# Optimization experiments

Measured on AMD Instinct MI355X. Metric: run time of the kernel, lower is better.

The kernel has to match this reference:

```python
import jax, jax.numpy as jnp
import numpy as np

H = 32          # num_attention_heads
HD = 128        # head_dim
HID = H * HD    # hidden_size = 4096
KB_LEN = 1024   # number of KB entries
TOPK = 128      # top_k_kb (dynamic_sparsify=True)
ROPE_THETA = 10000.0
PAD = -1000000000.0  # PADDING_VALUE


def rope_cos_sin(position_ids, head_dim, theta):
    inv_freq = 1.0 / (theta ** (jnp.arange(0, head_dim, 2, dtype=jnp.float32) / head_dim))
    freqs = position_ids.astype(jnp.float32)[..., None] * inv_freq  # [B,q,hd/2]
    emb = jnp.concatenate([freqs, freqs], axis=-1)                  # [B,q,hd]
    return jnp.cos(emb), jnp.sin(emb)


def rotate_half(x):
    half = x.shape[-1] // 2
    return jnp.concatenate([-x[..., half:], x[..., :half]], axis=-1)


def apply_rope(q, k, cos, sin):
    cos = cos[:, None]  # [B,1,q,hd]
    sin = sin[:, None]
    return q * cos + rotate_half(q) * sin, k * cos + rotate_half(k) * sin


def setup_inputs() -> dict:
    key = jax.random.key(0)
    ks = jax.random.split(key, 9)
    B, Q = 1, 2048
    w_scale = 0.02  # keep activations numerically sane
    hidden_states = jax.random.normal(ks[0], (B, Q, HID), jnp.float32)
    causal = jnp.where(jnp.tril(jnp.ones((Q, Q), bool)), 0.0, PAD).astype(jnp.float32)
    attention_mask = jnp.broadcast_to(causal[None, None], (B, 1, Q, Q))
    position_ids = jnp.broadcast_to(jnp.arange(Q)[None], (B, Q))
    kb_keys = jax.random.normal(ks[1], (KB_LEN, HID), jnp.float32)
    kb_values = jax.random.normal(ks[2], (KB_LEN, HID), jnp.float32)
    Wq = jax.random.normal(ks[3], (HID, HID), jnp.float32) * w_scale
    Wq2 = jax.random.normal(ks[4], (HID, HID), jnp.float32) * w_scale
    Wk = jax.random.normal(ks[5], (HID, HID), jnp.float32) * w_scale
    Wv = jax.random.normal(ks[6], (HID, HID), jnp.float32) * w_scale
    Wo = jax.random.normal(ks[7], (HID, HID), jnp.float32) * w_scale
    score_shift = jnp.zeros((H, 1), jnp.float32) - 3.0
    return {"hidden_states": hidden_states, "attention_mask": attention_mask,
            "position_ids": position_ids, "kb_keys": kb_keys, "kb_values": kb_values,
            "Wq": Wq, "Wq2": Wq2, "Wk": Wk, "Wv": Wv, "Wo": Wo,
            "score_shift": score_shift}


def kblam_attention(hidden_states, attention_mask, position_ids, kb_keys, kb_values,
                    Wq, Wq2, Wk, Wv, Wo, score_shift):
    B, Q, _ = hidden_states.shape
    scale = 1.0 / np.sqrt(HD)

    def heads(x):  # [B,Q,HID] -> [B,H,Q,HD]
        return x.reshape(B, Q, H, HD).transpose(0, 2, 1, 3)

    q = heads(hidden_states @ Wq.T)
    q2 = heads(hidden_states @ Wq2.T)   # second query head (used for KB top-k pruning)
    k = heads(hidden_states @ Wk.T)
    v = heads(hidden_states @ Wv.T)

    cos, sin = rope_cos_sin(position_ids, HD, ROPE_THETA)
    q, k = apply_rope(q, k, cos, sin)   # num_kv_groups == 1, repeat_kv is identity

    # --- KB path: [kb_len, H*HD] -> [B,H,kb_len,HD] ---
    kbk = jnp.broadcast_to(kb_keys.reshape(KB_LEN, H, HD).transpose(1, 0, 2)[None], (B, H, KB_LEN, HD))
    kbv = jnp.broadcast_to(kb_values.reshape(KB_LEN, H, HD).transpose(1, 0, 2)[None], (B, H, KB_LEN, HD))

    # prune_key_value (dynamic_sparsify): top-k KB rows by summed q2-scores
    aw2 = jnp.einsum('bhqd,bhkd->bhqk', q2, kbk) * scale          # [B,H,Q,KB_LEN]
    idx = jax.lax.stop_gradient(jax.lax.top_k(aw2.sum((1, 2)), TOPK)[1])  # [B,TOPK]
    gidx = jnp.broadcast_to(idx[:, None, :, None], (B, H, TOPK, HD))
    kbk = jnp.take_along_axis(kbk, gidx, axis=2)                  # [B,H,TOPK,HD]
    kbv = jnp.take_along_axis(kbv, gidx, axis=2)
    kb_len = TOPK

    k_all = jnp.concatenate([kbk, k], axis=2)                     # [B,H,kb_len+Q,HD]
    v_all = jnp.concatenate([kbv, v], axis=2)

    # kb attention mask: zeros, except fully-padded query rows get PADDING_VALUE
    padding_mask = jnp.all(attention_mask < 0, axis=-1, keepdims=True)  # [B,1,Q,1]
    kb_mask = jnp.where(padding_mask, PAD, 0.0).astype(attention_mask.dtype)
    mask = jnp.concatenate([jnp.broadcast_to(kb_mask, (B, 1, Q, kb_len)), attention_mask], axis=-1)

    attn = jnp.einsum('bhqd,bhkd->bhqk', q, k_all) * scale
    # learned per-head shift on KB scores (score_shift: [H,1], init -3)
    attn = attn.at[..., :kb_len].add(score_shift.reshape(1, H, 1, 1))
    attn = attn + mask
    attn = jax.nn.softmax(attn.astype(jnp.float32), axis=-1).astype(q.dtype)

    out = jnp.einsum('bhqk,bhkd->bhqd', attn, v_all)              # [B,H,Q,HD]
    out = out.transpose(0, 2, 1, 3).reshape(B, Q, HID)
    return out @ Wo.T


def reference(hidden_states, attention_mask, position_ids, kb_keys, kb_values,
              Wq, Wq2, Wk, Wv, Wo, score_shift):
    return kblam_attention(hidden_states, attention_mask, position_ids, kb_keys, kb_values,
                           Wq, Wq2, Wk, Wv, Wo, score_shift)
```

## Files before the change

kernel.cpp:

```cpp
#include <hip/hip_runtime.h>
#include <stdint.h>
#include <stddef.h>

#define NH 32
#define HD 128
#define HID 4096
#define QLEN 2048
#define KBLEN 1024
#define NTOPK 128
#define KVLEN 2176
#define PADV -1e9f
#define SCALE 0.08838834764831845f
#define LOG2E 1.4426950408889634f
#define SC2 (SCALE * LOG2E)
#define DEFER_THR 8.0f

typedef __attribute__((ext_vector_type(4))) float f32x4;
typedef __attribute__((ext_vector_type(4))) unsigned short u16x4;
typedef __attribute__((ext_vector_type(8))) short s16x8;

typedef const __attribute__((address_space(1))) void* gas1_t;
typedef __attribute__((address_space(3))) void* las3_t;

__device__ __forceinline__ void gload_lds16(const void* g, void* l) {
  __builtin_amdgcn_global_load_lds((gas1_t)g, (las3_t)l, 16, 0, 0);
}

__device__ __forceinline__ unsigned short f2bf(float x) {
  union { float f; unsigned u; } z; z.f = x;
  unsigned r = z.u + 0x7fffu + ((z.u >> 16) & 1u);
  return (unsigned short)(r >> 16);
}


__global__ void k_cast(const float* __restrict__ src, unsigned short* __restrict__ dst, int n4) {
  int i = blockIdx.x * 256 + threadIdx.x;
  if (i >= n4) return;
  f32x4 v = ((const f32x4*)src)[i];
  u16x4 o;
  o[0] = f2bf(v[0]); o[1] = f2bf(v[1]); o[2] = f2bf(v[2]); o[3] = f2bf(v[3]);
  ((u16x4*)dst)[i] = o;
}

__global__ void k_cast2(const float* __restrict__ s0, const float* __restrict__ s1,
                        unsigned short* __restrict__ d0, unsigned short* __restrict__ d1,
                        int n4each) {
  int i = blockIdx.x * 256 + threadIdx.x;
  int grp = (i >= n4each);
  const float* s = grp ? s1 : s0;
  unsigned short* d = grp ? d1 : d0;
  int j = grp ? (i - n4each) : i;
  f32x4 v = ((const f32x4*)s)[j];
  u16x4 o;
  o[0] = f2bf(v[0]); o[1] = f2bf(v[1]); o[2] = f2bf(v[2]); o[3] = f2bf(v[3]);
  ((u16x4*)d)[j] = o;
}

__global__ void k_rowsum_p(const float* __restrict__ x, float* __restrict__ part) {
  int d = blockIdx.x * 256 + threadIdx.x;
  int q0 = blockIdx.y * 128;
  float acc = 0.f;
  for (int q = q0; q < q0 + 128; ++q) acc += x[(size_t)q * HID + d];
  part[(size_t)blockIdx.y * HID + d] = acc;
}
__global__ void k_rowsum_r(const float* __restrict__ part, float* __restrict__ out) {
  int d = blockIdx.x * 256 + threadIdx.x;
  float acc = 0.f;
#pragma unroll
  for (int i = 0; i < 16; ++i) acc += part[(size_t)i * HID + d];
  out[d] = acc;
}

__global__ void k_dotrows(const float* __restrict__ vec, const float* __restrict__ mat,
                          float* __restrict__ out, int K, float s) {
  int n = blockIdx.x * 4 + (threadIdx.x >> 6);
  int lane = threadIdx.x & 63;
  const float* row = mat + (size_t)n * K;
  float acc = 0.f;
  for (int j = lane; j < K; j += 64) acc += vec[j] * row[j];
#pragma unroll
  for (int off = 32; off > 0; off >>= 1) acc += __shfl_down(acc, off, 64);
  if (lane == 0) out[n] = acc * s;
}

__global__ void k_topk(const float* __restrict__ scores, int* __restrict__ idx) {
  __shared__ float s[KBLEN];
  int t = threadIdx.x;
  s[t] = scores[t];
  __syncthreads();
  float mine = s[t];
  int rank = 0;
  for (int j = 0; j < KBLEN; ++j) {
    float v = s[j];
    rank += (v > mine) || (v == mine && j < t);
  }
  if (rank < NTOPK) idx[rank] = t;
}

__global__ void k_cs(const int* __restrict__ pos_ids, float2* __restrict__ cs) {
  int t = blockIdx.x * 256 + threadIdx.x;
  int p = t >> 6, i = t & 63;
  float pos = (float)pos_ids[p];
  float invf = powf(10000.0f, -(float)i / 64.0f);
  float a = pos * invf;
  cs[p * 64 + i] = make_float2(cosf(a), sinf(a));
}

__global__ void k_gather(const float* __restrict__ kbk, const float* __restrict__ kbv,
                         const int* __restrict__ idx,
                         unsigned short* __restrict__ kall, unsigned short* __restrict__ vallT) {
  int t = blockIdx.x * 256 + threadIdx.x;
  int d = t & 127;
  int i = (t >> 7) & 127;
  int hh = t >> 14;
  int kr = idx[i];
  size_t src = (size_t)kr * HID + hh * HD + d;
  kall[((size_t)hh * KVLEN + i) * HD + d] = f2bf(kbk[src]);
  vallT[((size_t)hh * HD + d) * KVLEN + i] = f2bf(kbv[src]);
}

#define GBK 64
#define ABUF 8192
#define BBUF 16384
#define BUFE (ABUF + BBUF)

#define GEMM_MAIN_LOOP                                                         \
  f32x4 acc[4][4] = {};                                                        \
  stageA(0, 0, 0); stageA(0, 0, 1);                                            \
  stageB(0, 0, 0); stageB(0, 0, 1); stageB(0, 0, 2); stageB(0, 0, 3);          \
  stageA(1, BUFE, 0); stageA(1, BUFE, 1);                                      \
  stageB(1, BUFE, 0); stageB(1, BUFE, 1); stageB(1, BUFE, 2); stageB(1, BUFE, 3); \
  const int NT = K / GBK;                                                      \
  const int sa = (lo & 7) << 3;                                                \
  const int bbase = (wn >> 1) * 128 + (wn & 1) * 32;                           \
  int bi = 0;                                                                  \
  for (int kt = 0; kt < NT; ++kt) {                                            \
    if (kt < NT - 1) { asm volatile("s_waitcnt vmcnt(6)" ::: "memory"); }      \
    else             { asm volatile("s_waitcnt vmcnt(0)" ::: "memory"); }      \
    __builtin_amdgcn_sched_barrier(0);                                         \
    __builtin_amdgcn_s_barrier();                                              \
    __builtin_amdgcn_sched_barrier(0);                                         \
    const int bufe = bi * BUFE;                                                \
    const int nbufe = ((bi + 2 >= 3) ? bi - 1 : bi + 2) * BUFE;                \
    const bool pre = (kt + 2 < NT);                                            \
    const unsigned short* Ab = lds + bufe;                                     \
    const unsigned short* Bb = lds + bufe + ABUF;                              \
    const int arow = wm * 64 + lo;                                             \
    const int brow = bbase + lo;                                               \
    s16x8 af[4], b01[2], b23[2];                                               \
    const int c0 = (hi * 8) ^ sa;                                              \
    const int c1 = (32 + hi * 8) ^ sa;                                         \
    _Pragma("unroll")                                                          \
    for (int i = 0; i < 4; ++i) af[i] = *(const s16x8*)(Ab + (arow + i * 16) * 64 + c0); \
    b01[0] = *(const s16x8*)(Bb + (brow +  0) * 64 + c0);                      \
    b01[1] = *(const s16x8*)(Bb + (brow + 16) * 64 + c0);                      \
    if (pre) { stageA(kt + 2, nbufe, 0); stageA(kt + 2, nbufe, 1); }           \
    asm volatile("s_waitcnt lgkmcnt(0)" ::: "memory");                         \
    __builtin_amdgcn_sched_barrier(0);                                         \
    __builtin_amdgcn_s_setprio(1);                                             \
    _Pragma("unroll")                                                          \
    for (int i = 0; i < 4; ++i) {                                              \
      acc[i][0] = __builtin_amdgcn_mfma_f32_16x16x32_bf16(af[i], b01[0], acc[i][0], 0, 0, 0); \
      acc[i][1] = __builtin_amdgcn_mfma_f32_16x16x32_bf16(af[i], b01[1], acc[i][1], 0, 0, 0); \
    }                                                                          \
    __builtin_amdgcn_s_setprio(0);                                             \
    b23[0] = *(const s16x8*)(Bb + (brow + 64) * 64 + c0);                      \
    b23[1] = *(const s16x8*)(Bb + (brow + 80) * 64 + c0);                      \
    if (pre) { stageB(kt + 2, nbufe, 0); stageB(kt + 2, nbufe, 1); }           \
    asm volatile("s_waitcnt lgkmcnt(0)" ::: "memory");                         \
    __builtin_amdgcn_sched_barrier(0);                                         \
    __builtin_amdgcn_s_setprio(1);                                             \
    _Pragma("unroll")                                                          \
    for (int i = 0; i < 4; ++i) {                                              \
      acc[i][2] = __builtin_amdgcn_mfma_f32_16x16x32_bf16(af[i], b23[0], acc[i][2], 0, 0, 0); \
      acc[i][3] = __builtin_amdgcn_mfma_f32_16x16x32_bf16(af[i], b23[1], acc[i][3], 0, 0, 0); \
    }                                                                          \
    __builtin_amdgcn_s_setprio(0);                                             \
    _Pragma("unroll")                                                          \
    for (int i = 0; i < 4; ++i) af[i] = *(const s16x8*)(Ab + (arow + i * 16) * 64 + c1); \
    b01[0] = *(const s16x8*)(Bb + (brow +  0) * 64 + c1);                      \
    b01[1] = *(const s16x8*)(Bb + (brow + 16) * 64 + c1);                      \
    if (pre) { stageB(kt + 2, nbufe, 2); stageB(kt + 2, nbufe, 3); }           \
    asm volatile("s_waitcnt lgkmcnt(0)" ::: "memory");                         \
    __builtin_amdgcn_sched_barrier(0);                                         \
    __builtin_amdgcn_s_setprio(1);                                             \
    _Pragma("unroll")                                                          \
    for (int i = 0; i < 4; ++i) {                                              \
      acc[i][0] = __builtin_amdgcn_mfma_f32_16x16x32_bf16(af[i], b01[0], acc[i][0], 0, 0, 0); \
      acc[i][1] = __builtin_amdgcn_mfma_f32_16x16x32_bf16(af[i], b01[1], acc[i][1], 0, 0, 0); \
    }                                                                          \
    __builtin_amdgcn_s_setprio(0);                                             \
    b23[0] = *(const s16x8*)(Bb + (brow + 64) * 64 + c1);                      \
    b23[1] = *(const s16x8*)(Bb + (brow + 80) * 64 + c1);                      \
    asm volatile("s_waitcnt lgkmcnt(0)" ::: "memory");                         \
    __builtin_amdgcn_sched_barrier(0);                                         \
    __builtin_amdgcn_s_setprio(1);                                             \
    _Pragma("unroll")                                                          \
    for (int i = 0; i < 4; ++i) {                                              \
      acc[i][2] = __builtin_amdgcn_mfma_f32_16x16x32_bf16(af[i], b23[0], acc[i][2], 0, 0, 0); \
      acc[i][3] = __builtin_amdgcn_mfma_f32_16x16x32_bf16(af[i], b23[1], acc[i][3], 0, 0, 0); \
    }                                                                          \
    __builtin_amdgcn_s_setprio(0);                                             \
    bi = (bi + 1 == 3) ? 0 : bi + 1;                                           \
  }

template<int MODE>
__global__ __launch_bounds__(512)
void gemm_bt(const unsigned short* __restrict__ A, const unsigned short* __restrict__ B,
             float* __restrict__ Cf, unsigned short* __restrict__ Cb,
             int M, int N, int K, int RH, int RO, const float2* __restrict__ cs2,
             float qsc) {
  __shared__ unsigned short lds[3 * BUFE];
  const int tid = threadIdx.x;
  const int lane = tid & 63;
  const int wave = tid >> 6;
  const int lo = lane & 15, hi = lane >> 4;
  const int wm = wave >> 2, wn = wave & 3;

  const int nwg = gridDim.x * gridDim.y;
  const int orig = blockIdx.y * gridDim.x + blockIdx.x;
  const int wg = (orig & 7) * (nwg >> 3) + (orig >> 3);
  const int bx = wg % gridDim.x, by = wg / gridDim.x;
  const int m0 = by * 128, n0 = bx * 256;

  auto stageA = [&](int kt, int bufe, int g) {
    int j0 = g * 512 + wave * 64;
    int j = j0 + lane;
    int row = j >> 3, cb = j & 7;
    gload_lds16(A + (size_t)(m0 + row) * K + kt * GBK + ((cb ^ (row & 7)) << 3),
                (void*)(lds + bufe + j0 * 8));
  };
  auto stageB = [&](int kt, int bufe, int g) {
    int j0 = g * 512 + wave * 64;
    int j = j0 + lane;
    int row = j >> 3, cb = j & 7;
    gload_lds16(B + (size_t)(n0 + row) * K + kt * GBK + ((cb ^ (row & 7)) << 3),
                (void*)(lds + bufe + ABUF + j0 * 8));
  };

  GEMM_MAIN_LOOP

  if (MODE == 2) {
#pragma unroll
    for (int i = 0; i < 4; ++i) {
#pragma unroll
      for (int j = 0; j < 2; ++j) {
#pragma unroll
        for (int r = 0; r < 4; ++r) {
          int row = m0 + wm * 64 + i * 16 + hi * 4 + r;
          int col = n0 + bbase + j * 16 + lo;
          int hh = col >> 7, d = col & 127;
          float2 cp = cs2[row * 64 + d];
          float x1 = acc[i][j][r] * qsc, x2 = acc[i][j + 2][r] * qsc;
          size_t base = ((size_t)hh * RH + RO + row) * HD;
          Cb[base + d]      = f2bf(x1 * cp.x - x2 * cp.y);
          Cb[base + d + 64] = f2bf(x2 * cp.x + x1 * cp.y);
        }
      }
    }
  } else if (MODE == 3) {
#pragma unroll
    for (int i = 0; i < 4; ++i) {
#pragma unroll
      for (int j = 0; j < 4; ++j) {
        int rowb = m0 + wm * 64 + i * 16 + hi * 4;
        int col = n0 + bbase + (j >> 1) * 64 + (j & 1) * 16 + lo;
        int hh = col >> 7, d = col & 127;
        u16x4 o4;
#pragma unroll
        for (int r = 0; r < 4; ++r) o4[r] = f2bf(acc[i][j][r]);
        *(u16x4*)(Cb + ((size_t)hh * HD + d) * RH + RO + rowb) = o4;
      }
    }
  } else {
#pragma unroll
    for (int i = 0; i < 4; ++i) {
#pragma unroll
      for (int j = 0; j < 4; ++j) {
#pragma unroll
        for (int r = 0; r < 4; ++r) {
          int row = m0 + wm * 64 + i * 16 + hi * 4 + r;
          int col = n0 + bbase + (j >> 1) * 64 + (j & 1) * 16 + lo;
          float v = acc[i][j][r];
          if (MODE == 0) {
            Cf[(size_t)row * N + col] = v;
          } else {
            int hh = col >> 7, d = col & 127;
            Cb[((size_t)hh * RH + RO + row) * HD + d] = f2bf(v);
          }
        }
      }
    }
  }
}

__global__ __launch_bounds__(512)
void gemm_qk(const unsigned short* __restrict__ A,
             const unsigned short* __restrict__ B0, const unsigned short* __restrict__ B1,
             unsigned short* __restrict__ C0, unsigned short* __restrict__ C1,
             const float2* __restrict__ cs2) {
  __shared__ unsigned short lds[3 * BUFE];
  const int tid = threadIdx.x;
  const int lane = tid & 63;
  const int wave = tid >> 6;
  const int lo = lane & 15, hi = lane >> 4;
  const int wm = wave >> 2, wn = wave & 3;

  const int nwg = gridDim.x * gridDim.y;
  const int orig = blockIdx.y * gridDim.x + blockIdx.x;
  const int wg = (orig & 7) * (nwg >> 3) + (orig >> 3);
  const int grp = wg >> 8;
  const int rem = wg & 255;
  const int bx = rem & 15, by = rem >> 4;
  const int m0 = by * 128, n0 = bx * 256;

  const unsigned short* B = grp ? B1 : B0;
  unsigned short* Cb = grp ? C1 : C0;
  const float qsc = grp ? 1.0f : (float)SC2;
  const int RH = grp ? KVLEN : QLEN;
  const int RO = grp ? NTOPK : 0;
  const int K = HID;

  auto stageA = [&](int kt, int bufe, int g) {
    int j0 = g * 512 + wave * 64;
    int j = j0 + lane;
    int row = j >> 3, cb = j & 7;
    gload_lds16(A + (size_t)(m0 + row) * K + kt * GBK + ((cb ^ (row & 7)) << 3),
                (void*)(lds + bufe + j0 * 8));
  };
  auto stageB = [&](int kt, int bufe, int g) {
    int j0 = g * 512 + wave * 64;
    int j = j0 + lane;
    int row = j >> 3, cb = j & 7;
    gload_lds16(B + (size_t)(n0 + row) * K + kt * GBK + ((cb ^ (row & 7)) << 3),
                (void*)(lds + bufe + ABUF + j0 * 8));
  };

  GEMM_MAIN_LOOP

#pragma unroll
  for (int i = 0; i < 4; ++i) {
#pragma unroll
    for (int j = 0; j < 2; ++j) {
#pragma unroll
      for (int r = 0; r < 4; ++r) {
        int row = m0 + wm * 64 + i * 16 + hi * 4 + r;
        int col = n0 + bbase + j * 16 + lo;
        int hh = col >> 7, d = col & 127;
        float2 cp = cs2[row * 64 + d];
        float x1 = acc[i][j][r] * qsc, x2 = acc[i][j + 2][r] * qsc;
        size_t base = ((size_t)hh * RH + RO + row) * HD;
        Cb[base + d]      = f2bf(x1 * cp.x - x2 * cp.y);
        Cb[base + d + 64] = f2bf(x2 * cp.x + x1 * cp.y);
      }
    }
  }
}

__global__ __launch_bounds__(256)
void attn_kernel(const unsigned short* __restrict__ qh,
                 const unsigned short* __restrict__ kall,
                 const unsigned short* __restrict__ vallT,
                 const float* __restrict__ sshift,
                 unsigned short* __restrict__ ctx) {
  __shared__ __align__(1024) unsigned short Ks[64 * 128];
  __shared__ __align__(1024) unsigned short Vs[128 * 64];
  __shared__ __align__(16)  unsigned short Plds[4][16 * 72];

  int orig = blockIdx.y * 32 + blockIdx.x;
  int wgid = (orig & 7) * 128 + (orig >> 3);
  int h = wgid >> 5;
  int qc = 31 - (wgid & 31);

  const int tid = threadIdx.x;
  const int lane = tid & 63;
  const int wave = tid >> 6;
  const int lo = lane & 15;
  const int hi = lane >> 4;
  const float shiftL = sshift[h] * LOG2E;

  const unsigned short* kb = kall + (size_t)h * KVLEN * HD;
  const unsigned short* vtb = vallT + (size_t)h * HD * KVLEN;

  const int m0 = qc * 64;
  const int nt = qc + 3;
  const int qrow = m0 + wave * 16 + hi * 4;

  s16x8 qf[4];
  {
    const unsigned short* qp = qh + ((size_t)h * QLEN + m0 + wave * 16 + lo) * HD + hi * 8;
#pragma unroll
    for (int kc = 0; kc < 4; ++kc) qf[kc] = *(const s16x8*)(qp + kc * 32);
  }

  float m_run[4], l_part[4];
#pragma unroll
  for (int r = 0; r < 4; ++r) { m_run[r] = -1e30f; l_part[r] = 0.f; }
  f32x4 o[8] = {};

  for (int kt = 0; kt < nt; ++kt) {
    const unsigned short* kg = kb + (size_t)kt * 64 * HD;
    const unsigned short* vg = vtb + kt * 64;
    __syncthreads();
#pragma unroll
    for (int it = 0; it < 4; ++it) {
      int j0 = it * 256 + wave * 64;
      int j = j0 + lane;
      int row = j >> 4, cb = j & 15;
      gload_lds16(kg + row * 128 + ((cb ^ (row & 7)) * 8), (void*)(Ks + j0 * 8));
      int d = j >> 3, c = j & 7;
      gload_lds16(vg + (size_t)d * KVLEN + ((c ^ (d & 7)) << 3), (void*)(Vs + j0 * 8));
    }
    __syncthreads();

    f32x4 s[4] = {};
#pragma unroll
    for (int kc = 0; kc < 4; ++kc) {
#pragma unroll
      for (int g = 0; g < 4; ++g) {
        int key = g * 16 + lo;
        s16x8 kf = *(const s16x8*)(Ks + key * 128 + (((kc * 4 + hi) ^ (key & 7)) * 8));
        s[g] = __builtin_amdgcn_mfma_f32_16x16x32_bf16(qf[kc], kf, s[g], 0, 0, 0);
      }
    }

    if (kt < 2) {
#pragma unroll
      for (int g = 0; g < 4; ++g)
#pragma unroll
        for (int r = 0; r < 4; ++r) s[g][r] += shiftL;
    } else if (kt == nt - 1) {
      const int kvbase = kt * 64;
#pragma unroll
      for (int r = 0; r < 4; ++r) {
        int qr = qrow + r;
#pragma unroll
        for (int g = 0; g < 4; ++g) {
          int kv = kvbase + g * 16 + lo;
          s[g][r] = (kv - NTOPK > qr) ? PADV : s[g][r];
        }
      }
    }

    float mx[4];
    bool need = false;
#pragma unroll
    for (int r = 0; r < 4; ++r) {
      mx[r] = fmaxf(fmaxf(s[0][r], s[1][r]), fmaxf(s[2][r], s[3][r]));
      need = need || (mx[r] > m_run[r] + DEFER_THR);
    }
    if (__any((int)need)) {
#pragma unroll
      for (int off = 1; off < 16; off <<= 1)
#pragma unroll
        for (int r = 0; r < 4; ++r) mx[r] = fmaxf(mx[r], __shfl_xor(mx[r], off, 64));
#pragma unroll
      for (int r = 0; r < 4; ++r) {
        float mn = fmaxf(m_run[r], mx[r]);
        float alpha = __builtin_amdgcn_exp2f(m_run[r] - mn);
        m_run[r] = mn;
        l_part[r] *= alpha;
#pragma unroll
        for (int db = 0; db < 8; ++db) o[db][r] *= alpha;
      }
    }

#pragma unroll
    for (int r = 0; r < 4; ++r) {
#pragma unroll
      for (int g = 0; g < 4; ++g) {
        float p = __builtin_amdgcn_exp2f(s[g][r] - m_run[r]);
        l_part[r] += p;
        Plds[wave][(hi * 4 + r) * 72 + g * 16 + lo] = f2bf(p);
      }
    }

    s16x8 pf0 = *(const s16x8*)(&Plds[wave][lo * 72 + hi * 8]);
    s16x8 pf1 = *(const s16x8*)(&Plds[wave][lo * 72 + 32 + hi * 8]);
#pragma unroll
    for (int db = 0; db < 8; ++db) {
      int d = db * 16 + lo;
      s16x8 vf0 = *(const s16x8*)(Vs + d * 64 + ((hi       ^ (d & 7)) << 3));
      s16x8 vf1 = *(const s16x8*)(Vs + d * 64 + (((4 + hi) ^ (d & 7)) << 3));
      o[db] = __builtin_amdgcn_mfma_f32_16x16x32_bf16(pf0, vf0, o[db], 0, 0, 0);
      o[db] = __builtin_amdgcn_mfma_f32_16x16x32_bf16(pf1, vf1, o[db], 0, 0, 0);
    }
  }

#pragma unroll
  for (int off = 1; off < 16; off <<= 1)
#pragma unroll
    for (int r = 0; r < 4; ++r) l_part[r] += __shfl_xor(l_part[r], off, 64);

  float rinv[4];
#pragma unroll
  for (int r = 0; r < 4; ++r) rinv[r] = __builtin_amdgcn_rcpf(l_part[r]);

#pragma unroll
  for (int db = 0; db < 8; ++db) {
#pragma unroll
    for (int r = 0; r < 4; ++r) {
      int row = qrow + r;
      int col = h * HD + db * 16 + lo;
      ctx[(size_t)row * HID + col] = f2bf(o[db][r] * rinv[r]);
    }
  }
}


extern "C" void kernel_launch(void* const* d_in, const int* in_sizes, int n_in,
                              void* d_out, int out_size, void* d_ws, size_t ws_size,
                              hipStream_t stream) {
  const float* hidden    = (const float*)d_in[0];
  const int*   pos       = (const int*)d_in[2];
  const float* kb_keys   = (const float*)d_in[3];
  const float* kb_values = (const float*)d_in[4];
  const float* Wq        = (const float*)d_in[5];
  const float* Wq2       = (const float*)d_in[6];
  const float* Wk        = (const float*)d_in[7];
  const float* Wv        = (const float*)d_in[8];
  const float* Wo        = (const float*)d_in[9];
  const float* sshift    = (const float*)d_in[10];
  float* out = (float*)d_out;

  char* ws = (char*)d_ws;
  size_t off = 0;
  auto alloc = [&](size_t bytes) { char* p = ws + off; off += (bytes + 255) & ~(size_t)255; return p; };
  unsigned short* hidden_bf = (unsigned short*)alloc((size_t)QLEN * HID * 2);
  unsigned short* wbuf      = (unsigned short*)alloc((size_t)HID * HID * 2);
  unsigned short* qbf       = (unsigned short*)alloc((size_t)NH * QLEN * HD * 2);
  unsigned short* kallp     = (unsigned short*)alloc((size_t)NH * KVLEN * HD * 2);
  unsigned short* vallT     = (unsigned short*)alloc((size_t)NH * HD * KVLEN * 2);
  unsigned short* ctx       = (unsigned short*)alloc((size_t)QLEN * HID * 2);
  float2*         cs2       = (float2*)alloc((size_t)QLEN * 64 * 8);
  float*          part      = (float*)alloc((size_t)16 * HID * 4);
  float*          hsum      = (float*)alloc(HID * 4);
  float*          qs        = (float*)alloc(HID * 4);
  float*          scores    = (float*)alloc(KBLEN * 4);
  int*            idx       = (int*)alloc(NTOPK * 4);

  unsigned short* wkbuf = (unsigned short*)out;

  dim3 blk(256);

  k_cast<<<QLEN * HID / 4 / 256, blk, 0, stream>>>(hidden, hidden_bf, QLEN * HID / 4);
  k_rowsum_p<<<dim3(HID / 256, 16), blk, 0, stream>>>(hidden, part);
  k_rowsum_r<<<HID / 256, blk, 0, stream>>>(part, hsum);
  k_dotrows<<<HID / 4, blk, 0, stream>>>(hsum, Wq2, qs, HID, 1.0f);
  k_dotrows<<<KBLEN / 4, blk, 0, stream>>>(qs, kb_keys, scores, HID, SCALE);
  k_topk<<<1, KBLEN, 0, stream>>>(scores, idx);
  k_cs<<<QLEN * 64 / 256, blk, 0, stream>>>(pos, cs2);

  dim3 ggrid(HID / 256, QLEN / 128);
  dim3 gblk(512);
  int wcast_blocks = HID * HID / 4 / 256;

  k_cast2<<<2 * wcast_blocks, blk, 0, stream>>>(Wq, Wk, wbuf, wkbuf, HID * HID / 4);
  dim3 qkgrid(16, 32);
  gemm_qk<<<qkgrid, gblk, 0, stream>>>(hidden_bf, wbuf, wkbuf, qbf, kallp, cs2);

  k_cast<<<wcast_blocks, blk, 0, stream>>>(Wv, wbuf, HID * HID / 4);
  gemm_bt<3><<<ggrid, gblk, 0, stream>>>(hidden_bf, wbuf, nullptr, vallT, QLEN, HID, HID, KVLEN, NTOPK, cs2, 1.0f);

  k_gather<<<NH * NTOPK * HD / 256, blk, 0, stream>>>(kb_keys, kb_values, idx, kallp, vallT);

  dim3 agrid(32, NH);
  attn_kernel<<<agrid, blk, 0, stream>>>(qbf, kallp, vallT, sshift, ctx);

  k_cast<<<wcast_blocks, blk, 0, stream>>>(Wo, wbuf, HID * HID / 4);
  gemm_bt<0><<<ggrid, gblk, 0, stream>>>(ctx, wbuf, out, nullptr, QLEN, HID, HID, 0, 0, cs2, 1.0f);
}
```

Measured before the change: 561.7 us.

## Fuse V projection into QK GEMM and cast all four weights in one launch

Extends the combined Q/K GEMM to a third group that computes the V projection, writing V transposed into the padded KV buffer, so Q, K and V run as one 768-workgroup launch. All four weight matrices are cast to bf16 in a single kernel into separate workspace buffers, removing two cast launches and one GEMM launch. The merged GEMM has a larger grid, which can help the tail and fill the device better. The cost is extra workspace for separate Wv and Wo bf16 copies, and the output-projection weight cast now happens before attention instead of right before use.

```diff
diff --git a/kernel.cpp b/kernel.cpp
--- a/kernel.cpp
+++ b/kernel.cpp
@@ -42,14 +42,16 @@
   ((u16x4*)dst)[i] = o;
 }
 
-__global__ void k_cast2(const float* __restrict__ s0, const float* __restrict__ s1,
+__global__ void k_cast4(const float* __restrict__ s0, const float* __restrict__ s1,
+                        const float* __restrict__ s2, const float* __restrict__ s3,
                         unsigned short* __restrict__ d0, unsigned short* __restrict__ d1,
+                        unsigned short* __restrict__ d2, unsigned short* __restrict__ d3,
                         int n4each) {
   int i = blockIdx.x * 256 + threadIdx.x;
-  int grp = (i >= n4each);
-  const float* s = grp ? s1 : s0;
-  unsigned short* d = grp ? d1 : d0;
-  int j = grp ? (i - n4each) : i;
+  int grp = i / n4each;
+  int j = i - grp * n4each;
+  const float* s = (grp == 0) ? s0 : (grp == 1) ? s1 : (grp == 2) ? s2 : s3;
+  unsigned short* d = (grp == 0) ? d0 : (grp == 1) ? d1 : (grp == 2) ? d2 : d3;
   f32x4 v = ((const f32x4*)s)[j];
   u16x4 o;
   o[0] = f2bf(v[0]); o[1] = f2bf(v[1]); o[2] = f2bf(v[2]); o[3] = f2bf(v[3]);
@@ -240,65 +242,33 @@
 
   GEMM_MAIN_LOOP
 
-  if (MODE == 2) {
-#pragma unroll
-    for (int i = 0; i < 4; ++i) {
-#pragma unroll
-      for (int j = 0; j < 2; ++j) {
-#pragma unroll
-        for (int r = 0; r < 4; ++r) {
-          int row = m0 + wm * 64 + i * 16 + hi * 4 + r;
-          int col = n0 + bbase + j * 16 + lo;
+#pragma unroll
+  for (int i = 0; i < 4; ++i) {
+#pragma unroll
+    for (int j = 0; j < 4; ++j) {
+#pragma unroll
+      for (int r = 0; r < 4; ++r) {
+        int row = m0 + wm * 64 + i * 16 + hi * 4 + r;
+        int col = n0 + bbase + (j >> 1) * 64 + (j & 1) * 16 + lo;
+        float v = acc[i][j][r];
+        if (MODE == 0) {
+          Cf[(size_t)row * N + col] = v;
+        } else {
           int hh = col >> 7, d = col & 127;
-          float2 cp = cs2[row * 64 + d];
-          float x1 = acc[i][j][r] * qsc, x2 = acc[i][j + 2][r] * qsc;
-          size_t base = ((size_t)hh * RH + RO + row) * HD;
-          Cb[base + d]      = f2bf(x1 * cp.x - x2 * cp.y);
-          Cb[base + d + 64] = f2bf(x2 * cp.x + x1 * cp.y);
+          Cb[((size_t)hh * RH + RO + row) * HD + d] = f2bf(v);
         }
       }
     }
-  } else if (MODE == 3) {
-#pragma unroll
-    for (int i = 0; i < 4; ++i) {
-#pragma unroll
-      for (int j = 0; j < 4; ++j) {
-        int rowb = m0 + wm * 64 + i * 16 + hi * 4;
-        int col = n0 + bbase + (j >> 1) * 64 + (j & 1) * 16 + lo;
-        int hh = col >> 7, d = col & 127;
-        u16x4 o4;
-#pragma unroll
-        for (int r = 0; r < 4; ++r) o4[r] = f2bf(acc[i][j][r]);
-        *(u16x4*)(Cb + ((size_t)hh * HD + d) * RH + RO + rowb) = o4;
-      }
-    }
-  } else {
-#pragma unroll
-    for (int i = 0; i < 4; ++i) {
-#pragma unroll
-      for (int j = 0; j < 4; ++j) {
-#pragma unroll
-        for (int r = 0; r < 4; ++r) {
-          int row = m0 + wm * 64 + i * 16 + hi * 4 + r;
-          int col = n0 + bbase + (j >> 1) * 64 + (j & 1) * 16 + lo;
-          float v = acc[i][j][r];
-          if (MODE == 0) {
-            Cf[(size_t)row * N + col] = v;
-          } else {
-            int hh = col >> 7, d = col & 127;
-            Cb[((size_t)hh * RH + RO + row) * HD + d] = f2bf(v);
-          }
-        }
-      }
-    }
   }
 }
 
 __global__ __launch_bounds__(512)
-void gemm_qk(const unsigned short* __restrict__ A,
-             const unsigned short* __restrict__ B0, const unsigned short* __restrict__ B1,
-             unsigned short* __restrict__ C0, unsigned short* __restrict__ C1,
-             const float2* __restrict__ cs2) {
+void gemm_qkv(const unsigned short* __restrict__ A,
+              const unsigned short* __restrict__ B0, const unsigned short* __restrict__ B1,
+              const unsigned short* __restrict__ B2,
+              unsigned short* __restrict__ C0, unsigned short* __restrict__ C1,
+              unsigned short* __restrict__ C2,
+              const float2* __restrict__ cs2) {
   __shared__ unsigned short lds[3 * BUFE];
   const int tid = threadIdx.x;
   const int lane = tid & 63;
@@ -314,11 +284,7 @@
   const int bx = rem & 15, by = rem >> 4;
   const int m0 = by * 128, n0 = bx * 256;
 
-  const unsigned short* B = grp ? B1 : B0;
-  unsigned short* Cb = grp ? C1 : C0;
-  const float qsc = grp ? 1.0f : (float)SC2;
-  const int RH = grp ? KVLEN : QLEN;
-  const int RO = grp ? NTOPK : 0;
+  const unsigned short* B = (grp == 0) ? B0 : (grp == 1) ? B1 : B2;
   const int K = HID;
 
   auto stageA = [&](int kt, int bufe, int g) {
@@ -338,20 +304,40 @@
 
   GEMM_MAIN_LOOP
 
-#pragma unroll
-  for (int i = 0; i < 4; ++i) {
-#pragma unroll
-    for (int j = 0; j < 2; ++j) {
-#pragma unroll
-      for (int r = 0; r < 4; ++r) {
-        int row = m0 + wm * 64 + i * 16 + hi * 4 + r;
-        int col = n0 + bbase + j * 16 + lo;
+  if (grp < 2) {
+    unsigned short* Cb = grp ? C1 : C0;
+    const float qsc = grp ? 1.0f : (float)SC2;
+    const int RH = grp ? KVLEN : QLEN;
+    const int RO = grp ? NTOPK : 0;
+#pragma unroll
+    for (int i = 0; i < 4; ++i) {
+#pragma unroll
+      for (int j = 0; j < 2; ++j) {
+#pragma unroll
+        for (int r = 0; r < 4; ++r) {
+          int row = m0 + wm * 64 + i * 16 + hi * 4 + r;
+          int col = n0 + bbase + j * 16 + lo;
+          int hh = col >> 7, d = col & 127;
+          float2 cp = cs2[row * 64 + d];
+          float x1 = acc[i][j][r] * qsc, x2 = acc[i][j + 2][r] * qsc;
+          size_t base = ((size_t)hh * RH + RO + row) * HD;
+          Cb[base + d]      = f2bf(x1 * cp.x - x2 * cp.y);
+          Cb[base + d + 64] = f2bf(x2 * cp.x + x1 * cp.y);
+        }
+      }
+    }
+  } else {
+#pragma unroll
+    for (int i = 0; i < 4; ++i) {
+#pragma unroll
+      for (int j = 0; j < 4; ++j) {
+        int rowb = m0 + wm * 64 + i * 16 + hi * 4;
+        int col = n0 + bbase + (j >> 1) * 64 + (j & 1) * 16 + lo;
         int hh = col >> 7, d = col & 127;
-        float2 cp = cs2[row * 64 + d];
-        float x1 = acc[i][j][r] * qsc, x2 = acc[i][j + 2][r] * qsc;
-        size_t base = ((size_t)hh * RH + RO + row) * HD;
-        Cb[base + d]      = f2bf(x1 * cp.x - x2 * cp.y);
-        Cb[base + d + 64] = f2bf(x2 * cp.x + x1 * cp.y);
+        u16x4 o4;
+#pragma unroll
+        for (int r = 0; r < 4; ++r) o4[r] = f2bf(acc[i][j][r]);
+        *(u16x4*)(C2 + ((size_t)hh * HD + d) * KVLEN + NTOPK + rowb) = o4;
       }
     }
   }
@@ -528,6 +514,8 @@
   auto alloc = [&](size_t bytes) { char* p = ws + off; off += (bytes + 255) & ~(size_t)255; return p; };
   unsigned short* hidden_bf = (unsigned short*)alloc((size_t)QLEN * HID * 2);
   unsigned short* wbuf      = (unsigned short*)alloc((size_t)HID * HID * 2);
+  unsigned short* wvbuf     = (unsigned short*)alloc((size_t)HID * HID * 2);
+  unsigned short* wobuf     = (unsigned short*)alloc((size_t)HID * HID * 2);
   unsigned short* qbf       = (unsigned short*)alloc((size_t)NH * QLEN * HD * 2);
   unsigned short* kallp     = (unsigned short*)alloc((size_t)NH * KVLEN * HD * 2);
   unsigned short* vallT     = (unsigned short*)alloc((size_t)NH * HD * KVLEN * 2);
@@ -542,6 +530,7 @@
   unsigned short* wkbuf = (unsigned short*)out;
 
   dim3 blk(256);
+  int wcast_blocks = HID * HID / 4 / 256;
 
   k_cast<<<QLEN * HID / 4 / 256, blk, 0, stream>>>(hidden, hidden_bf, QLEN * HID / 4);
   k_rowsum_p<<<dim3(HID / 256, 16), blk, 0, stream>>>(hidden, part);
@@ -551,22 +540,20 @@
   k_topk<<<1, KBLEN, 0, stream>>>(scores, idx);
   k_cs<<<QLEN * 64 / 256, blk, 0, stream>>>(pos, cs2);
 
-  dim3 ggrid(HID / 256, QLEN / 128);
+  k_cast4<<<4 * wcast_blocks, blk, 0, stream>>>(Wq, Wk, Wv, Wo,
+                                                wbuf, wkbuf, wvbuf, wobuf,
+                                                HID * HID / 4);
+
   dim3 gblk(512);
-  int wcast_blocks = HID * HID / 4 / 256;
-
-  k_cast2<<<2 * wcast_blocks, blk, 0, stream>>>(Wq, Wk, wbuf, wkbuf, HID * HID / 4);
-  dim3 qkgrid(16, 32);
-  gemm_qk<<<qkgrid, gblk, 0, stream>>>(hidden_bf, wbuf, wkbuf, qbf, kallp, cs2);
-
-  k_cast<<<wcast_blocks, blk, 0, stream>>>(Wv, wbuf, HID * HID / 4);
-  gemm_bt<3><<<ggrid, gblk, 0, stream>>>(hidden_bf, wbuf, nullptr, vallT, QLEN, HID, HID, KVLEN, NTOPK, cs2, 1.0f);
+  dim3 qkvgrid(16, 48);
+  gemm_qkv<<<qkvgrid, gblk, 0, stream>>>(hidden_bf, wbuf, wkbuf, wvbuf,
+                                         qbf, kallp, vallT, cs2);
 
   k_gather<<<NH * NTOPK * HD / 256, blk, 0, stream>>>(kb_keys, kb_values, idx, kallp, vallT);
 
   dim3 agrid(32, NH);
   attn_kernel<<<agrid, blk, 0, stream>>>(qbf, kallp, vallT, sshift, ctx);
 
-  k_cast<<<wcast_blocks, blk, 0, stream>>>(Wo, wbuf, HID * HID / 4);
-  gemm_bt<0><<<ggrid, gblk, 0, stream>>>(ctx, wbuf, out, nullptr, QLEN, HID, HID, 0, 0, cs2, 1.0f);
-}
+  dim3 ggrid(HID / 256, QLEN / 128);
+  gemm_bt<0><<<ggrid, gblk, 0, stream>>>(ctx, wobuf, out, nullptr, QLEN, HID, HID, 0, 0, cs2, 1.0f);
+}
```

Result: no change. 554.1 us (-1.3%).
